# Performance work log

Measured on AMD Instinct MI355X. Metric: run time of the kernel, lower is better.

The kernel has to match this reference:

```python
import jax, jax.numpy as jnp
import numpy as np

SCALE_REACH = 10.0   # 'scale' in forward
SCALE_COS = 16.0     # CosNorm_Classifier default scale


def setup_inputs() -> dict:
    key = jax.random.key(0)
    ks = jax.random.split(key, 7)
    B, C, F = 64, 1000, 2048
    return {
        "x": jax.random.normal(ks[0], (B, F), jnp.float32),
        "centroids": jax.random.normal(ks[1], (C, F), jnp.float32),
        "W_hall": jax.random.normal(ks[2], (C, F), jnp.float32) * 0.02,
        "b_hall": jax.random.normal(ks[3], (C,), jnp.float32) * 0.02,
        "W_sel": jax.random.normal(ks[4], (F, F), jnp.float32) * 0.02,
        "b_sel": jax.random.normal(ks[5], (F,), jnp.float32) * 0.02,
        "W_cos": jax.random.normal(ks[6], (C, F), jnp.float32) * 0.001,
    }


def reference(x, centroids, W_hall, b_hall, W_sel, b_sel, W_cos):
    direct_feature = x
    # L2 distance to every class centroid: [B, C] (materializes [B, C, F] diff as in torch)
    diff = x[:, None, :] - centroids[None, :, :]
    dist = jnp.sqrt(jnp.sum(diff * diff, axis=2))
    # original sorts then takes column 0 -> min distance
    min_dist = jnp.min(dist, axis=1)                      # [B]
    reachability = (SCALE_REACH / min_dist)[:, None]      # [B, 1], broadcast over feat

    # hallucinated memory read
    values_memory = jax.nn.softmax(x @ W_hall.T + b_hall, axis=1)  # [B, C]
    memory_feature = values_memory @ centroids                      # [B, F]

    concept_selector = jnp.tanh(x @ W_sel.T + b_sel)                # [B, F]
    infused_feature = concept_selector * memory_feature
    feat = reachability * (direct_feature + infused_feature)

    # CosNorm classifier
    norm_x = jnp.linalg.norm(feat, axis=1, keepdims=True)           # [B, 1]
    ex = (norm_x / (1.0 + norm_x)) * (feat / norm_x)                # norm-gated unit vec
    ew = W_cos / jnp.linalg.norm(W_cos, axis=1, keepdims=True)      # [C, F]
    logits = ex @ (ew.T * SCALE_COS)                                # [B, C]

    return logits, direct_feature, infused_feature
```

## Files before the change

### kernel.cpp

```cpp
#include <hip/hip_runtime.h>
#include <math.h>

#define FF 2048

typedef __attribute__((ext_vector_type(8))) short short8;
typedef __attribute__((ext_vector_type(4))) float floatx4;

#define OFF_SPART 0
#define OFF_HPART 1024000
#define OFF_SELP  2048000
#define OFF_MEMP  3096576
#define OFF_LOGP  5193728
#define OFF_V     7241728
#define OFF_FEAT  7305728
#define OFF_CN2   7436800
#define OFF_WINV  7437800
#define OFF_XN2   7438800
#define OFF_REACH 7438864
#define OFF_NRM2P 7438928
#define OFF_CTR   7439488
#define OFF_FLAG  7440512

#define TP 40

__device__ __forceinline__ float cld(const float* p) {
  return __hip_atomic_load(p, __ATOMIC_RELAXED, __HIP_MEMORY_SCOPE_AGENT);
}
__device__ __forceinline__ void cst(float* p, float v) {
  __hip_atomic_store(p, v, __ATOMIC_RELAXED, __HIP_MEMORY_SCOPE_AGENT);
}

__device__ __forceinline__ void split2(float f, ushort& h, ushort& l) {
  unsigned u = __float_as_uint(f);
  float r = f - __uint_as_float(u & 0xffff0000u);
  h = (ushort)(u >> 16);
  l = (ushort)(__float_as_uint(r) >> 16);
}

__device__ __forceinline__ void stage_bt_bf(const float* __restrict__ M, int ldK, int rowBase,
                                            int nrows, int k0, int kmax,
                                            ushort* __restrict__ hi, ushort* __restrict__ lo, int t) {
  int r = t >> 2, q = t & 3;
  int grow = rowBase + r;
  bool rok = grow < nrows;
  const float* src = M + (size_t)grow * ldK + k0 + q * 8;
#pragma unroll
  for (int h = 0; h < 2; ++h) {
    int kb = k0 + q * 8 + h * 4;
    float4 v = make_float4(0.f, 0.f, 0.f, 0.f);
    if (rok) {
      if (kb + 3 < kmax) {
        v = *(const float4*)(src + h * 4);
      } else {
#pragma unroll
        for (int j = 0; j < 4; ++j)
          if (kb + j < kmax) ((float*)&v)[j] = src[h * 4 + j];
      }
    }
    ushort4 hv, lv;
    split2(v.x, hv.x, lv.x); split2(v.y, hv.y, lv.y);
    split2(v.z, hv.z, lv.z); split2(v.w, hv.w, lv.w);
    int base = r * TP + q * 8 + h * 4;
    *(ushort4*)(hi + base) = hv;
    *(ushort4*)(lo + base) = lv;
  }
}

__device__ __forceinline__ void stage_bt_coh(const float* __restrict__ M, int ldK,
                                             int k0, int kmax,
                                             ushort* __restrict__ hi, ushort* __restrict__ lo, int t) {
  int r = t >> 2, q = t & 3;
  const float* src = M + (size_t)r * ldK + k0 + q * 8;
#pragma unroll
  for (int h = 0; h < 2; ++h) {
    float v[4];
#pragma unroll
    for (int j = 0; j < 4; ++j) {
      int kk = k0 + q * 8 + h * 4 + j;
      v[j] = (kk < kmax) ? cld(src + h * 4 + j) : 0.f;
    }
    ushort4 hv, lv;
    split2(v[0], hv.x, lv.x); split2(v[1], hv.y, lv.y);
    split2(v[2], hv.z, lv.z); split2(v[3], hv.w, lv.w);
    int base = r * TP + q * 8 + h * 4;
    *(ushort4*)(hi + base) = hv;
    *(ushort4*)(lo + base) = lv;
  }
}

__device__ __forceinline__ void stage_tr_bf(const float* __restrict__ M, int ldN, int k0, int kmax,
                                            int n0, ushort* __restrict__ hi, ushort* __restrict__ lo, int t) {
  int kk = t >> 3, c8 = (t & 7) * 8;
  int gk = k0 + kk;
  const float* src = M + (size_t)gk * ldN + n0 + c8;
  float4 v0 = make_float4(0.f, 0.f, 0.f, 0.f), v1 = v0;
  if (gk < kmax) { v0 = *(const float4*)src; v1 = *(const float4*)(src + 4); }
#pragma unroll
  for (int j = 0; j < 8; ++j) {
    float f = (j < 4) ? ((float*)&v0)[j] : ((float*)&v1)[j - 4];
    ushort h, l;
    split2(f, h, l);
    hi[(c8 + j) * TP + kk] = h;
    lo[(c8 + j) * TP + kk] = l;
  }
}

#define MFMA(a, b, c) __builtin_amdgcn_mfma_f32_16x16x32_bf16(a, b, c, 0, 0, 0)

#define NBLK 512

__device__ __forceinline__ void gbar(unsigned* __restrict__ ctr, unsigned* __restrict__ flag,
                                     unsigned phase) {
  __syncthreads();
  int t = threadIdx.x;
  if (t == 0)
    __hip_atomic_fetch_add(ctr + (blockIdx.x & 63) * 16, 1u, __ATOMIC_RELAXED, __HIP_MEMORY_SCOPE_AGENT);
  if (blockIdx.x == 0) {
    if (t < 64) {
      unsigned target = (unsigned)NBLK * phase;
      for (;;) {
        unsigned v = __hip_atomic_load(ctr + t * 16, __ATOMIC_RELAXED, __HIP_MEMORY_SCOPE_AGENT);
#pragma unroll
        for (int off = 32; off > 0; off >>= 1) v += __shfl_down(v, off, 64);
        v = __shfl(v, 0, 64);
        if (v >= target) break;
        __builtin_amdgcn_s_sleep(1);
      }
      if (t == 0)
        __hip_atomic_store(flag + phase * 16, 1u, __ATOMIC_RELAXED, __HIP_MEMORY_SCOPE_AGENT);
    }
  } else {
    if (t == 0) {
      while (__hip_atomic_load(flag + phase * 16, __ATOMIC_RELAXED, __HIP_MEMORY_SCOPE_AGENT) == 0u)
        __builtin_amdgcn_s_sleep(2);
    }
  }
  __syncthreads();
}

__global__ void k_init(unsigned* ctr) {
  int t = threadIdx.x;
#pragma unroll
  for (int i = 0; i < 5; ++i)
    __hip_atomic_store(ctr + i * 256 + t, 0u, __ATOMIC_RELAXED, __HIP_MEMORY_SCOPE_AGENT);
}

__global__ __launch_bounds__(256) void k_all(
    const float* __restrict__ x, const float* __restrict__ cent,
    const float* __restrict__ whall, const float* __restrict__ bhall,
    const float* __restrict__ wsel, const float* __restrict__ bsel,
    const float* __restrict__ wcos, float* __restrict__ ws, float* __restrict__ out) {
  __shared__ __align__(16) char smem[6 * 64 * TP * 2];
  ushort* Ah  = (ushort*)smem;
  ushort* Al  = Ah + 64 * TP;
  ushort* B1h = Ah + 2 * 64 * TP;
  ushort* B1l = Ah + 3 * 64 * TP;
  ushort* B2h = Ah + 4 * 64 * TP;
  ushort* B2l = Ah + 5 * 64 * TP;
  float* hrow = (float*)smem;
  float* red  = (float*)smem + 1000;

  int bx = blockIdx.x, t = threadIdx.x;
  int lane = t & 63, w = t >> 6;
  int ln15 = t & 15, lq = (t >> 4) & 3, q8 = lq * 8;
  int mh = w & 1, nh = w >> 1;
  unsigned* ctr  = (unsigned*)(ws + OFF_CTR);
  unsigned* flag = (unsigned*)(ws + OFF_FLAG);

  for (int r = bx * 4 + w; r < 2064; r += 2048) {
    const float* src = (r < 1000) ? cent + (size_t)r * FF
                     : (r < 2000) ? wcos + (size_t)(r - 1000) * FF
                                  : x + (size_t)(r - 2000) * FF;
    float s = 0.f;
#pragma unroll
    for (int i = 0; i < 8; ++i) {
      float4 v = *(const float4*)(src + i * 256 + lane * 4);
      s += v.x * v.x + v.y * v.y + v.z * v.z + v.w * v.w;
    }
#pragma unroll
    for (int off = 32; off > 0; off >>= 1) s += __shfl_down(s, off, 64);
    if (lane == 0) {
      if (r < 1000) cst(ws + OFF_CN2 + r, s);
      else if (r < 2000) cst(ws + OFF_WINV + (r - 1000), 1.f / sqrtf(s));
      else cst(ws + OFF_XN2 + (r - 2000), s);
    }
  }

  if (bx < 256) {
    int tile = bx & 15, ks = bx >> 4;
    int n0 = tile * 64;
    floatx4 accS[2][2], accH[2][2];
#pragma unroll
    for (int i = 0; i < 2; ++i)
#pragma unroll
      for (int j = 0; j < 2; ++j) { accS[i][j] = (floatx4){0.f,0.f,0.f,0.f}; accH[i][j] = (floatx4){0.f,0.f,0.f,0.f}; }
    for (int kc = 0; kc < 4; ++kc) {
      int k0 = ks * 128 + kc * 32;
      __syncthreads();
      stage_bt_bf(x,     FF, 0,  64,   k0, FF, Ah,  Al,  t);
      stage_bt_bf(cent,  FF, n0, 1000, k0, FF, B1h, B1l, t);
      stage_bt_bf(whall, FF, n0, 1000, k0, FF, B2h, B2l, t);
      __syncthreads();
      short8 ah[2], al[2];
#pragma unroll
      for (int i = 0; i < 2; ++i) {
        int row = (mh * 2 + i) * 16 + ln15;
        ah[i] = *(const short8*)(Ah + row * TP + q8);
        al[i] = *(const short8*)(Al + row * TP + q8);
      }
#pragma unroll
      for (int j = 0; j < 2; ++j) {
        int brow = (nh * 2 + j) * 16 + ln15;
        short8 b1h = *(const short8*)(B1h + brow * TP + q8);
        short8 b1l = *(const short8*)(B1l + brow * TP + q8);
        short8 b2h = *(const short8*)(B2h + brow * TP + q8);
        short8 b2l = *(const short8*)(B2l + brow * TP + q8);
#pragma unroll
        for (int i = 0; i < 2; ++i) {
          accS[i][j] = MFMA(ah[i], b1h, accS[i][j]);
          accS[i][j] = MFMA(ah[i], b1l, accS[i][j]);
          accS[i][j] = MFMA(al[i], b1h, accS[i][j]);
          accH[i][j] = MFMA(ah[i], b2h, accH[i][j]);
          accH[i][j] = MFMA(ah[i], b2l, accH[i][j]);
          accH[i][j] = MFMA(al[i], b2h, accH[i][j]);
        }
      }
    }
    float* Spart = ws + OFF_SPART + (size_t)ks * 64000;
    float* Hpart = ws + OFF_HPART + (size_t)ks * 64000;
#pragma unroll
    for (int i = 0; i < 2; ++i)
#pragma unroll
      for (int j = 0; j < 2; ++j) {
        int gn = n0 + (nh * 2 + j) * 16 + ln15;
        if (gn < 1000) {
#pragma unroll
          for (int r = 0; r < 4; ++r) {
            int gm = (mh * 2 + i) * 16 + lq * 4 + r;
            cst(Spart + gm * 1000 + gn, accS[i][j][r]);
            cst(Hpart + gm * 1000 + gn, accH[i][j][r]);
          }
        }
      }
  } else {
    int b2 = bx - 256;
    int tile = b2 & 31, ks = b2 >> 5;
    int n0 = tile * 64;
    floatx4 acc[2][2];
#pragma unroll
    for (int i = 0; i < 2; ++i)
#pragma unroll
      for (int j = 0; j < 2; ++j) acc[i][j] = (floatx4){0.f,0.f,0.f,0.f};
    for (int kc = 0; kc < 8; ++kc) {
      int k0 = ks * 256 + kc * 32;
      __syncthreads();
      stage_bt_bf(x,    FF, 0,  64, k0, FF, Ah,  Al,  t);
      stage_bt_bf(wsel, FF, n0, FF, k0, FF, B1h, B1l, t);
      __syncthreads();
      short8 ah[2], al[2];
#pragma unroll
      for (int i = 0; i < 2; ++i) {
        int row = (mh * 2 + i) * 16 + ln15;
        ah[i] = *(const short8*)(Ah + row * TP + q8);
        al[i] = *(const short8*)(Al + row * TP + q8);
      }
#pragma unroll
      for (int j = 0; j < 2; ++j) {
        int brow = (nh * 2 + j) * 16 + ln15;
        short8 bh = *(const short8*)(B1h + brow * TP + q8);
        short8 bl = *(const short8*)(B1l + brow * TP + q8);
#pragma unroll
        for (int i = 0; i < 2; ++i) {
          acc[i][j] = MFMA(ah[i], bh, acc[i][j]);
          acc[i][j] = MFMA(ah[i], bl, acc[i][j]);
          acc[i][j] = MFMA(al[i], bh, acc[i][j]);
        }
      }
    }
    float* selp = ws + OFF_SELP + (size_t)ks * 131072;
#pragma unroll
    for (int i = 0; i < 2; ++i)
#pragma unroll
      for (int j = 0; j < 2; ++j) {
        int gn = n0 + (nh * 2 + j) * 16 + ln15;
#pragma unroll
        for (int r = 0; r < 4; ++r) {
          int gm = (mh * 2 + i) * 16 + lq * 4 + r;
          cst(selp + gm * 2048 + gn, acc[i][j][r]);
        }
      }
  }

  gbar(ctr, flag, 1);

  if (bx < 64) {
    int b = bx;
    const float* Spart = ws + OFF_SPART;
    const float* Hpart = ws + OFF_HPART;
    float xn = cld(ws + OFF_XN2 + b);
    float lmin = 3.0e38f, lmax = -3.0e38f;
    for (int c = t; c < 1000; c += 256) {
      float S = 0.f, H = 0.f;
#pragma unroll
      for (int ks = 0; ks < 16; ++ks) {
        S += cld(Spart + (size_t)ks * 64000 + b * 1000 + c);
        H += cld(Hpart + (size_t)ks * 64000 + b * 1000 + c);
      }
      H += bhall[c];
      hrow[c] = H;
      float d2 = xn - 2.f * S + cld(ws + OFF_CN2 + c);
      lmin = fminf(lmin, d2);
      lmax = fmaxf(lmax, H);
    }
    red[t] = lmin; __syncthreads();
    for (int s = 128; s > 0; s >>= 1) { if (t < s) red[t] = fminf(red[t], red[t + s]); __syncthreads(); }
    float bmin = red[0]; __syncthreads();
    red[t] = lmax; __syncthreads();
    for (int s = 128; s > 0; s >>= 1) { if (t < s) red[t] = fmaxf(red[t], red[t + s]); __syncthreads(); }
    float bmax = red[0]; __syncthreads();
    float lsum = 0.f;
    for (int c = t; c < 1000; c += 256) {
      float e = expf(hrow[c] - bmax);
      hrow[c] = e;
      lsum += e;
    }
    red[t] = lsum; __syncthreads();
    for (int s = 128; s > 0; s >>= 1) { if (t < s) red[t] += red[t + s]; __syncthreads(); }
    float inv = 1.f / red[0];
    float* V = ws + OFF_V;
    for (int c = t; c < 1000; c += 256) cst(V + b * 1000 + c, hrow[c] * inv);
    if (t == 0) cst(ws + OFF_REACH + b, 10.f / sqrtf(bmin));
  }

  gbar(ctr, flag, 2);

  {
    int tile = bx & 31, ks = bx >> 5;
    int n0 = tile * 64;
    const float* V = ws + OFF_V;
    floatx4 acc[2][2];
#pragma unroll
    for (int i = 0; i < 2; ++i)
#pragma unroll
      for (int j = 0; j < 2; ++j) acc[i][j] = (floatx4){0.f,0.f,0.f,0.f};
    for (int kc = 0; kc < 2; ++kc) {
      int k0 = ks * 64 + kc * 32;
      __syncthreads();
      stage_bt_coh(V, 1000, k0, 1000, Ah, Al, t);
      stage_tr_bf(cent, FF, k0, 1000, n0, B1h, B1l, t);
      __syncthreads();
      short8 ah[2], al[2];
#pragma unroll
      for (int i = 0; i < 2; ++i) {
        int row = (mh * 2 + i) * 16 + ln15;
        ah[i] = *(const short8*)(Ah + row * TP + q8);
        al[i] = *(const short8*)(Al + row * TP + q8);
      }
#pragma unroll
      for (int j = 0; j < 2; ++j) {
        int brow = (nh * 2 + j) * 16 + ln15;
        short8 bh = *(const short8*)(B1h + brow * TP + q8);
        short8 bl = *(const short8*)(B1l + brow * TP + q8);
#pragma unroll
        for (int i = 0; i < 2; ++i) {
          acc[i][j] = MFMA(ah[i], bh, acc[i][j]);
          acc[i][j] = MFMA(ah[i], bl, acc[i][j]);
          acc[i][j] = MFMA(al[i], bh, acc[i][j]);
        }
      }
    }
    float* memp = ws + OFF_MEMP + (size_t)ks * 131072;
#pragma unroll
    for (int i = 0; i < 2; ++i)
#pragma unroll
      for (int j = 0; j < 2; ++j) {
        int gn = n0 + (nh * 2 + j) * 16 + ln15;
#pragma unroll
        for (int r = 0; r < 4; ++r) {
          int gm = (mh * 2 + i) * 16 + lq * 4 + r;
          cst(memp + gm * 2048 + gn, acc[i][j][r]);
        }
      }
  }

  gbar(ctr, flag, 3);

  {
    int row = bx >> 3, chunk = bx & 7;
    int f = chunk * 256 + t;
    const float* selp = ws + OFF_SELP;
    const float* memp = ws + OFF_MEMP;
    float* feat = ws + OFF_FEAT;
    float rch = cld(ws + OFF_REACH + row);
    float sp = bsel[f], mm = 0.f;
#pragma unroll
    for (int ks = 0; ks < 8; ++ks) sp += cld(selp + (size_t)ks * 131072 + row * 2048 + f);
#pragma unroll
    for (int ks = 0; ks < 16; ++ks) mm += cld(memp + (size_t)ks * 131072 + row * 2048 + f);
    float sel = tanhf(sp);
    float inf = sel * mm;
    float xv = x[row * 2048 + f];
    float ft = rch * (xv + inf);
    out[64000 + row * 2048 + f] = xv;
    out[195072 + row * 2048 + f] = inf;
    cst(feat + row * 2048 + f, ft);
    float nrm2 = ft * ft;
    __syncthreads();
    red[t] = nrm2; __syncthreads();
    for (int s = 128; s > 0; s >>= 1) { if (t < s) red[t] += red[t + s]; __syncthreads(); }
    if (t == 0) cst(ws + OFF_NRM2P + row * 8 + chunk, red[0]);
  }

  gbar(ctr, flag, 4);

  {
    int tile = bx & 15, ks = bx >> 4;
    int n0 = tile * 64;
    const float* feat = ws + OFF_FEAT;
    floatx4 acc[2][2];
#pragma unroll
    for (int i = 0; i < 2; ++i)
#pragma unroll
      for (int j = 0; j < 2; ++j) acc[i][j] = (floatx4){0.f,0.f,0.f,0.f};
    for (int kc = 0; kc < 2; ++kc) {
      int k0 = ks * 64 + kc * 32;
      __syncthreads();
      stage_bt_coh(feat, FF, k0, FF, Ah, Al, t);
      stage_bt_bf(wcos, FF, n0, 1000, k0, FF, B1h, B1l, t);
      __syncthreads();
      short8 ah[2], al[2];
#pragma unroll
      for (int i = 0; i < 2; ++i) {
        int row = (mh * 2 + i) * 16 + ln15;
        ah[i] = *(const short8*)(Ah + row * TP + q8);
        al[i] = *(const short8*)(Al + row * TP + q8);
      }
#pragma unroll
      for (int j = 0; j < 2; ++j) {
        int brow = (nh * 2 + j) * 16 + ln15;
        short8 bh = *(const short8*)(B1h + brow * TP + q8);
        short8 bl = *(const short8*)(B1l + brow * TP + q8);
#pragma unroll
        for (int i = 0; i < 2; ++i) {
          acc[i][j] = MFMA(ah[i], bh, acc[i][j]);
          acc[i][j] = MFMA(ah[i], bl, acc[i][j]);
          acc[i][j] = MFMA(al[i], bh, acc[i][j]);
        }
      }
    }
    float* logp = ws + OFF_LOGP + (size_t)ks * 64000;
#pragma unroll
    for (int i = 0; i < 2; ++i)
#pragma unroll
      for (int j = 0; j < 2; ++j) {
        int gn = n0 + (nh * 2 + j) * 16 + ln15;
        if (gn < 1000) {
#pragma unroll
          for (int r = 0; r < 4; ++r) {
            int gm = (mh * 2 + i) * 16 + lq * 4 + r;
            cst(logp + gm * 1000 + gn, acc[i][j][r]);
          }
        }
      }
  }

  gbar(ctr, flag, 5);

  if (t < 125) {
    int idx = bx * 125 + t;
    const float* logp = ws + OFF_LOGP;
    float s = 0.f;
#pragma unroll
    for (int ks = 0; ks < 32; ++ks) s += cld(logp + (size_t)ks * 64000 + idx);
    int b = idx / 1000;
    int c = idx - b * 1000;
    float n2 = 0.f;
#pragma unroll
    for (int q = 0; q < 8; ++q) n2 += cld(ws + OFF_NRM2P + b * 8 + q);
    float sfac = 16.f / (1.f + sqrtf(n2));
    out[idx] = s * sfac * cld(ws + OFF_WINV + c);
  }
}

extern "C" void kernel_launch(void* const* d_in, const int* in_sizes, int n_in,
                              void* d_out, int out_size, void* d_ws, size_t ws_size,
                              hipStream_t stream) {
  const float* x     = (const float*)d_in[0];
  const float* cent  = (const float*)d_in[1];
  const float* whall = (const float*)d_in[2];
  const float* bhall = (const float*)d_in[3];
  const float* wsel  = (const float*)d_in[4];
  const float* bsel  = (const float*)d_in[5];
  const float* wcos  = (const float*)d_in[6];
  float* out = (float*)d_out;
  float* ws  = (float*)d_ws;
  unsigned* ctr = (unsigned*)(ws + OFF_CTR);

  hipLaunchKernelGGL(k_init, dim3(1), dim3(256), 0, stream, ctr);
  hipLaunchKernelGGL(k_all, dim3(NBLK), dim3(256), 0, stream,
                     x, cent, whall, bhall, wsel, bsel, wcos, ws, out);
}
```

Before: 139.5 us.

## Distribute softmax/distance reduction across all blocks and vectorize coherent partial-sum loads

The per-row softmax and min-distance phase, previously done by only 64 blocks, is now split across all 512 blocks. Each block writes chunk-level min, max and exp-sum partials, and a small extra phase combines them into a per-row max, inverse sum and reachability. The softmax exponentiation is moved into the staging of the memory-read GEMM. The coherent scalar loads in the reduction phases are replaced with inline-asm dwordx4 loads and stores that use sc0/sc1 bits and batched waits. This adds one more grid barrier in exchange for more parallelism and fewer, wider memory operations.

Result: faster. 136.3 us (-2.3%).

```diff
diff --git a/kernel.cpp b/kernel.cpp
--- a/kernel.cpp
+++ b/kernel.cpp
@@ -11,15 +11,16 @@
 #define OFF_SELP  2048000
 #define OFF_MEMP  3096576
 #define OFF_LOGP  5193728
-#define OFF_V     7241728
-#define OFF_FEAT  7305728
-#define OFF_CN2   7436800
-#define OFF_WINV  7437800
-#define OFF_XN2   7438800
-#define OFF_REACH 7438864
-#define OFF_NRM2P 7438928
-#define OFF_CTR   7439488
-#define OFF_FLAG  7440512
+#define OFF_HROW  7241728
+#define OFF_FEAT  7307264
+#define OFF_CN2   7438336
+#define OFF_WINV  7439336
+#define OFF_XN2   7440336
+#define OFF_MM    7440400
+#define OFF_ROWF  7442448
+#define OFF_NRM2P 7442704
+#define OFF_CTR   7443216
+#define OFF_FLAG  7444240
 
 #define TP 40
 
@@ -28,6 +29,28 @@
 }
 __device__ __forceinline__ void cst(float* p, float v) {
   __hip_atomic_store(p, v, __ATOMIC_RELAXED, __HIP_MEMORY_SCOPE_AGENT);
+}
+__device__ __forceinline__ floatx4 cld4(const float* p) {
+  floatx4 d;
+  asm volatile("global_load_dwordx4 %0, %1, off sc0 sc1\n\ts_waitcnt vmcnt(0)"
+               : "=&v"(d) : "v"(p) : "memory");
+  return d;
+}
+__device__ __forceinline__ void cld4x4(const float* p0, const float* p1,
+                                       const float* p2, const float* p3,
+                                       floatx4& a, floatx4& b, floatx4& c, floatx4& d) {
+  asm volatile(
+      "global_load_dwordx4 %0, %4, off sc0 sc1\n\t"
+      "global_load_dwordx4 %1, %5, off sc0 sc1\n\t"
+      "global_load_dwordx4 %2, %6, off sc0 sc1\n\t"
+      "global_load_dwordx4 %3, %7, off sc0 sc1\n\t"
+      "s_waitcnt vmcnt(0)"
+      : "=&v"(a), "=&v"(b), "=&v"(c), "=&v"(d)
+      : "v"(p0), "v"(p1), "v"(p2), "v"(p3)
+      : "memory");
+}
+__device__ __forceinline__ void cst4(float* p, floatx4 v) {
+  asm volatile("global_store_dwordx4 %0, %1, off sc0 sc1" :: "v"(p), "v"(v) : "memory");
 }
 
 __device__ __forceinline__ void split2(float f, ushort& h, ushort& l) {
@@ -66,19 +89,32 @@
   }
 }
 
-__device__ __forceinline__ void stage_bt_coh(const float* __restrict__ M, int ldK,
-                                             int k0, int kmax,
-                                             ushort* __restrict__ hi, ushort* __restrict__ lo, int t) {
+__device__ __forceinline__ void stage_v(const float* __restrict__ hrowg, float gm, float inv,
+                                        int k0, ushort* __restrict__ hi, ushort* __restrict__ lo, int t) {
   int r = t >> 2, q = t & 3;
-  const float* src = M + (size_t)r * ldK + k0 + q * 8;
 #pragma unroll
   for (int h = 0; h < 2; ++h) {
+    int kb = k0 + q * 8 + h * 4;
+    floatx4 hv4 = cld4(hrowg + (size_t)r * 1024 + kb);
     float v[4];
 #pragma unroll
-    for (int j = 0; j < 4; ++j) {
-      int kk = k0 + q * 8 + h * 4 + j;
-      v[j] = (kk < kmax) ? cld(src + h * 4 + j) : 0.f;
-    }
+    for (int j = 0; j < 4; ++j)
+      v[j] = (kb + j < 1000) ? expf(hv4[j] - gm) * inv : 0.f;
+    ushort4 hv, lv;
+    split2(v[0], hv.x, lv.x); split2(v[1], hv.y, lv.y);
+    split2(v[2], hv.z, lv.z); split2(v[3], hv.w, lv.w);
+    int base = r * TP + q * 8 + h * 4;
+    *(ushort4*)(hi + base) = hv;
+    *(ushort4*)(lo + base) = lv;
+  }
+}
+
+__device__ __forceinline__ void stage_feat4(const float* __restrict__ feat, int k0,
+                                            ushort* __restrict__ hi, ushort* __restrict__ lo, int t) {
+  int r = t >> 2, q = t & 3;
+#pragma unroll
+  for (int h = 0; h < 2; ++h) {
+    floatx4 v = cld4(feat + (size_t)r * 2048 + k0 + q * 8 + h * 4);
     ushort4 hv, lv;
     split2(v[0], hv.x, lv.x); split2(v[1], hv.y, lv.y);
     split2(v[2], hv.z, lv.z); split2(v[3], hv.w, lv.w);
@@ -111,6 +147,7 @@
 
 __device__ __forceinline__ void gbar(unsigned* __restrict__ ctr, unsigned* __restrict__ flag,
                                      unsigned phase) {
+  asm volatile("s_waitcnt vmcnt(0)" ::: "memory");
   __syncthreads();
   int t = threadIdx.x;
   if (t == 0)
@@ -157,8 +194,7 @@
   ushort* B1l = Ah + 3 * 64 * TP;
   ushort* B2h = Ah + 4 * 64 * TP;
   ushort* B2l = Ah + 5 * 64 * TP;
-  float* hrow = (float*)smem;
-  float* red  = (float*)smem + 1000;
+  float* red2 = (float*)smem;
 
   int bx = blockIdx.x, t = threadIdx.x;
   int lane = t & 63, w = t >> 6;
@@ -293,51 +329,104 @@
 
   gbar(ctr, flag, 1);
 
-  if (bx < 64) {
-    int b = bx;
-    const float* Spart = ws + OFF_SPART;
-    const float* Hpart = ws + OFF_HPART;
-    float xn = cld(ws + OFF_XN2 + b);
-    float lmin = 3.0e38f, lmax = -3.0e38f;
-    for (int c = t; c < 1000; c += 256) {
-      float S = 0.f, H = 0.f;
-#pragma unroll
-      for (int ks = 0; ks < 16; ++ks) {
-        S += cld(Spart + (size_t)ks * 64000 + b * 1000 + c);
-        H += cld(Hpart + (size_t)ks * 64000 + b * 1000 + c);
-      }
-      H += bhall[c];
-      hrow[c] = H;
-      float d2 = xn - 2.f * S + cld(ws + OFF_CN2 + c);
-      lmin = fminf(lmin, d2);
-      lmax = fmaxf(lmax, H);
-    }
-    red[t] = lmin; __syncthreads();
-    for (int s = 128; s > 0; s >>= 1) { if (t < s) red[t] = fminf(red[t], red[t + s]); __syncthreads(); }
-    float bmin = red[0]; __syncthreads();
-    red[t] = lmax; __syncthreads();
-    for (int s = 128; s > 0; s >>= 1) { if (t < s) red[t] = fmaxf(red[t], red[t + s]); __syncthreads(); }
-    float bmax = red[0]; __syncthreads();
-    float lsum = 0.f;
-    for (int c = t; c < 1000; c += 256) {
-      float e = expf(hrow[c] - bmax);
-      hrow[c] = e;
-      lsum += e;
-    }
-    red[t] = lsum; __syncthreads();
-    for (int s = 128; s > 0; s >>= 1) { if (t < s) red[t] += red[t + s]; __syncthreads(); }
-    float inv = 1.f / red[0];
-    float* V = ws + OFF_V;
-    for (int c = t; c < 1000; c += 256) cst(V + b * 1000 + c, hrow[c] * inv);
-    if (t == 0) cst(ws + OFF_REACH + b, 10.f / sqrtf(bmin));
+  {
+    int b = bx >> 3, ch = bx & 7;
+    int g = t >> 5, ci = t & 31;
+    int c = ch * 128 + ci * 4;
+    const float* Sp  = ws + OFF_SPART + (size_t)g * 64000 + b * 1000 + c;
+    const float* Hp  = ws + OFF_HPART + (size_t)g * 64000 + b * 1000 + c;
+    floatx4 s1, s2, h1, h2;
+    cld4x4(Sp, Sp + 8 * 64000, Hp, Hp + 8 * 64000, s1, s2, h1, h2);
+    float S4[4], H4[4];
+#pragma unroll
+    for (int j = 0; j < 4; ++j) {
+      S4[j] = s1[j] + s2[j];
+      H4[j] = h1[j] + h2[j];
+    }
+#pragma unroll
+    for (int j = 0; j < 4; ++j) {
+      red2[(g * 32 + ci) * 8 + j]     = S4[j];
+      red2[(g * 32 + ci) * 8 + 4 + j] = H4[j];
+    }
+    __syncthreads();
+    if (t < 32) {
+      float S[4] = {0,0,0,0}, H[4] = {0,0,0,0};
+#pragma unroll
+      for (int g2 = 0; g2 < 8; ++g2)
+#pragma unroll
+        for (int j = 0; j < 4; ++j) {
+          S[j] += red2[(g2 * 32 + t) * 8 + j];
+          H[j] += red2[(g2 * 32 + t) * 8 + 4 + j];
+        }
+      int c0 = ch * 128 + t * 4;
+      float xn = cld(ws + OFF_XN2 + b);
+      float Hf[4], lmin = 3.0e38f, lmax = -3.0e38f;
+#pragma unroll
+      for (int j = 0; j < 4; ++j) {
+        bool valid = (c0 + j) < 1000;
+        float bh = valid ? bhall[c0 + j] : 0.f;
+        Hf[j] = valid ? (H[j] + bh) : -3.0e38f;
+        float cn = valid ? cld(ws + OFF_CN2 + c0 + j) : 0.f;
+        float d2 = valid ? (xn - 2.f * S[j] + cn) : 3.0e38f;
+        lmin = fminf(lmin, d2);
+        lmax = fmaxf(lmax, Hf[j]);
+      }
+      cst4(ws + OFF_HROW + b * 1024 + c0, (floatx4){Hf[0], Hf[1], Hf[2], Hf[3]});
+      float cmin = lmin, cmax = lmax;
+#pragma unroll
+      for (int off = 16; off > 0; off >>= 1) {
+        cmin = fminf(cmin, __shfl_down(cmin, off, 32));
+        cmax = fmaxf(cmax, __shfl_down(cmax, off, 32));
+      }
+      cmin = __shfl(cmin, 0, 32);
+      cmax = __shfl(cmax, 0, 32);
+      float lsum = 0.f;
+#pragma unroll
+      for (int j = 0; j < 4; ++j)
+        if ((c0 + j) < 1000) lsum += expf(Hf[j] - cmax);
+#pragma unroll
+      for (int off = 16; off > 0; off >>= 1) lsum += __shfl_down(lsum, off, 32);
+      if (t == 0) {
+        float* mm = ws + OFF_MM + (b * 8 + ch) * 4;
+        cst(mm + 0, cmin);
+        cst(mm + 1, cmax);
+        cst(mm + 2, lsum);
+      }
+    }
   }
 
   gbar(ctr, flag, 2);
+
+  if (bx < 64 && t < 8) {
+    const float* mm = ws + OFF_MM + (bx * 8 + t) * 4;
+    float mn = cld(mm + 0), mx = cld(mm + 1), sm = cld(mm + 2);
+    float gmin = mn, gmax = mx;
+#pragma unroll
+    for (int off = 4; off > 0; off >>= 1) {
+      gmin = fminf(gmin, __shfl_down(gmin, off, 8));
+      gmax = fmaxf(gmax, __shfl_down(gmax, off, 8));
+    }
+    gmin = __shfl(gmin, 0, 8);
+    gmax = __shfl(gmax, 0, 8);
+    float dp = sm * expf(mx - gmax);
+#pragma unroll
+    for (int off = 4; off > 0; off >>= 1) dp += __shfl_down(dp, off, 8);
+    if (t == 0) {
+      float* rf = ws + OFF_ROWF + bx * 4;
+      cst(rf + 0, gmax);
+      cst(rf + 1, 1.f / dp);
+      cst(rf + 2, 10.f / sqrtf(gmin));
+    }
+  }
+
+  gbar(ctr, flag, 3);
 
   {
     int tile = bx & 31, ks = bx >> 5;
     int n0 = tile * 64;
-    const float* V = ws + OFF_V;
+    int vr = t >> 2;
+    float gm  = cld(ws + OFF_ROWF + vr * 4 + 0);
+    float inv = cld(ws + OFF_ROWF + vr * 4 + 1);
     floatx4 acc[2][2];
 #pragma unroll
     for (int i = 0; i < 2; ++i)
@@ -346,7 +435,7 @@
     for (int kc = 0; kc < 2; ++kc) {
       int k0 = ks * 64 + kc * 32;
       __syncthreads();
-      stage_bt_coh(V, 1000, k0, 1000, Ah, Al, t);
+      stage_v(ws + OFF_HROW, gm, inv, k0, Ah, Al, t);
       stage_tr_bf(cent, FF, k0, 1000, n0, B1h, B1l, t);
       __syncthreads();
       short8 ah[2], al[2];
@@ -377,46 +466,68 @@
         int gn = n0 + (nh * 2 + j) * 16 + ln15;
 #pragma unroll
         for (int r = 0; r < 4; ++r) {
-          int gm = (mh * 2 + i) * 16 + lq * 4 + r;
-          cst(memp + gm * 2048 + gn, acc[i][j][r]);
-        }
-      }
-  }
-
-  gbar(ctr, flag, 3);
-
-  {
-    int row = bx >> 3, chunk = bx & 7;
-    int f = chunk * 256 + t;
-    const float* selp = ws + OFF_SELP;
-    const float* memp = ws + OFF_MEMP;
-    float* feat = ws + OFF_FEAT;
-    float rch = cld(ws + OFF_REACH + row);
-    float sp = bsel[f], mm = 0.f;
-#pragma unroll
-    for (int ks = 0; ks < 8; ++ks) sp += cld(selp + (size_t)ks * 131072 + row * 2048 + f);
-#pragma unroll
-    for (int ks = 0; ks < 16; ++ks) mm += cld(memp + (size_t)ks * 131072 + row * 2048 + f);
-    float sel = tanhf(sp);
-    float inf = sel * mm;
-    float xv = x[row * 2048 + f];
-    float ft = rch * (xv + inf);
-    out[64000 + row * 2048 + f] = xv;
-    out[195072 + row * 2048 + f] = inf;
-    cst(feat + row * 2048 + f, ft);
-    float nrm2 = ft * ft;
-    __syncthreads();
-    red[t] = nrm2; __syncthreads();
-    for (int s = 128; s > 0; s >>= 1) { if (t < s) red[t] += red[t + s]; __syncthreads(); }
-    if (t == 0) cst(ws + OFF_NRM2P + row * 8 + chunk, red[0]);
+          int gm2 = (mh * 2 + i) * 16 + lq * 4 + r;
+          cst(memp + gm2 * 2048 + gn, acc[i][j][r]);
+        }
+      }
   }
 
   gbar(ctr, flag, 4);
+
+  if (t < 64) {
+    int row = bx >> 3, ch2 = bx & 7;
+    int f = ch2 * 256 + t * 4;
+    const float* selp = ws + OFF_SELP + (size_t)row * 2048 + f;
+    const float* memp = ws + OFF_MEMP + (size_t)row * 2048 + f;
+    floatx4 a0, a1, a2, a3;
+    float sp[4], mm4[4];
+    cld4x4(selp, selp + 131072, selp + 2 * 131072, selp + 3 * 131072, a0, a1, a2, a3);
+#pragma unroll
+    for (int j = 0; j < 4; ++j)
+      sp[j] = a0[j] + a1[j] + a2[j] + a3[j];
+    cld4x4(selp + 4 * 131072, selp + 5 * 131072, selp + 6 * 131072, selp + 7 * 131072, a0, a1, a2, a3);
+#pragma unroll
+    for (int j = 0; j < 4; ++j)
+      sp[j] += a0[j] + a1[j] + a2[j] + a3[j];
+#pragma unroll
+    for (int j = 0; j < 4; ++j) mm4[j] = 0.f;
+#pragma unroll
+    for (int q = 0; q < 4; ++q) {
+      cld4x4(memp + (size_t)(4 * q) * 131072, memp + (size_t)(4 * q + 1) * 131072,
+             memp + (size_t)(4 * q + 2) * 131072, memp + (size_t)(4 * q + 3) * 131072,
+             a0, a1, a2, a3);
+#pragma unroll
+      for (int j = 0; j < 4; ++j)
+        mm4[j] += a0[j] + a1[j] + a2[j] + a3[j];
+    }
+    float4 bs4 = *(const float4*)(bsel + f);
+    float4 x4  = *(const float4*)(x + (size_t)row * 2048 + f);
+    float rch = cld(ws + OFF_ROWF + row * 4 + 2);
+    float4 inf4;
+    floatx4 ft4;
+    float nrm2 = 0.f;
+#pragma unroll
+    for (int j = 0; j < 4; ++j) {
+      float sel = tanhf(sp[j] + ((float*)&bs4)[j]);
+      float inf = sel * mm4[j];
+      float ft = rch * (((float*)&x4)[j] + inf);
+      ((float*)&inf4)[j] = inf;
+      ft4[j] = ft;
+      nrm2 += ft * ft;
+    }
+    *(float4*)(out + 64000 + (size_t)row * 2048 + f) = x4;
+    *(float4*)(out + 195072 + (size_t)row * 2048 + f) = inf4;
+    cst4(ws + OFF_FEAT + (size_t)row * 2048 + f, ft4);
+#pragma unroll
+    for (int off = 32; off > 0; off >>= 1) nrm2 += __shfl_down(nrm2, off, 64);
+    if (t == 0) cst(ws + OFF_NRM2P + row * 8 + ch2, nrm2);
+  }
+
+  gbar(ctr, flag, 5);
 
   {
     int tile = bx & 15, ks = bx >> 4;
     int n0 = tile * 64;
-    const float* feat = ws + OFF_FEAT;
     floatx4 acc[2][2];
 #pragma unroll
     for (int i = 0; i < 2; ++i)
@@ -425,7 +536,7 @@
     for (int kc = 0; kc < 2; ++kc) {
       int k0 = ks * 64 + kc * 32;
       __syncthreads();
-      stage_bt_coh(feat, FF, k0, FF, Ah, Al, t);
+      stage_feat4(ws + OFF_FEAT, k0, Ah, Al, t);
       stage_bt_bf(wcos, FF, n0, 1000, k0, FF, B1h, B1l, t);
       __syncthreads();
       short8 ah[2], al[2];
@@ -464,21 +575,40 @@
       }
   }
 
-  gbar(ctr, flag, 5);
-
-  if (t < 125) {
-    int idx = bx * 125 + t;
-    const float* logp = ws + OFF_LOGP;
-    float s = 0.f;
-#pragma unroll
-    for (int ks = 0; ks < 32; ++ks) s += cld(logp + (size_t)ks * 64000 + idx);
-    int b = idx / 1000;
-    int c = idx - b * 1000;
-    float n2 = 0.f;
-#pragma unroll
-    for (int q = 0; q < 8; ++q) n2 += cld(ws + OFF_NRM2P + b * 8 + q);
-    float sfac = 16.f / (1.f + sqrtf(n2));
-    out[idx] = s * sfac * cld(ws + OFF_WINV + c);
+  gbar(ctr, flag, 6);
+
+  if (bx < 500 && t < 32) {
+    int idx0 = (bx * 32 + t) * 4;
+    const float* logp = ws + OFF_LOGP + idx0;
+    float s4[4] = {0,0,0,0};
+    floatx4 a0, a1, a2, a3;
+#pragma unroll
+    for (int q = 0; q < 8; ++q) {
+      cld4x4(logp + (size_t)(4 * q) * 64000, logp + (size_t)(4 * q + 1) * 64000,
+             logp + (size_t)(4 * q + 2) * 64000, logp + (size_t)(4 * q + 3) * 64000,
+             a0, a1, a2, a3);
+#pragma unroll
+      for (int j = 0; j < 4; ++j)
+        s4[j] += a0[j] + a1[j] + a2[j] + a3[j];
+    }
+    floatx4 o4;
+    int pb = -1;
+    float sfac = 0.f;
+#pragma unroll
+    for (int j = 0; j < 4; ++j) {
+      int idx = idx0 + j;
+      int bb = idx / 1000;
+      int cc = idx - bb * 1000;
+      if (bb != pb) {
+        float n2 = 0.f;
+#pragma unroll
+        for (int q = 0; q < 8; ++q) n2 += cld(ws + OFF_NRM2P + bb * 8 + q);
+        sfac = 16.f / (1.f + sqrtf(n2));
+        pb = bb;
+      }
+      o4[j] = s4[j] * sfac * cld(ws + OFF_WINV + cc);
+    }
+    *(floatx4*)(out + idx0) = o4;
   }
 }
 
```
